# Kernel tuning notes

Hardware: AMD Instinct MI355X
Metric: run time of the kernel (lower is better)

The kernel has to match this reference:

```python
import jax, jax.numpy as jnp
import numpy as np

B, H, FEAT = 16384, 256, 256
GX, GY, SW = 70, 70, 2


def setup_inputs() -> dict:
    key = jax.random.key(0)
    ks = jax.random.split(key, 10)
    stdv = 1.0 / np.sqrt(H)
    feats = jax.random.normal(ks[0], (B, FEAT), dtype=jnp.float32)
    coords = jax.random.randint(ks[1], (B, 2), 0, 64).astype(jnp.float32)
    input_tensor = jnp.concatenate([feats, coords], axis=1)  # [B, FEAT+2]
    hidden = jax.random.normal(ks[2], (B, H), dtype=jnp.float32)
    u = lambda k, shp: jax.random.uniform(k, shp, jnp.float32, -stdv, stdv)
    return {
        "input_tensor": input_tensor,
        "hidden": hidden,
        "w_ih": u(ks[3], (4 * H, FEAT)),
        "b_ih": u(ks[4], (4 * H,)),
        "w_hh": u(ks[5], (4 * H, H)),
        "b_hh": u(ks[6], (4 * H,)),
        "w_out": u(ks[7], (H, 2 * H)),
        "b_out": u(ks[8], (H,)),
        "memory": jax.random.normal(ks[9], (GX, GY, H), dtype=jnp.float32) * 0.1,
    }


def reference(input_tensor, hidden, w_ih, b_ih, w_hh, b_hh, w_out, b_out, memory):
    feature = input_tensor[:, :-2]
    grid = input_tensor[:, -2:].astype(jnp.int32) + SW  # [B,2]

    gi = feature @ w_ih.T + b_ih  # [B,4H]
    gh = hidden @ w_hh.T + b_hh   # [B,4H]
    i_r, i_i, i_n, i_s = jnp.split(gi, 4, axis=1)
    h_r, h_i, h_n, h_s = jnp.split(gh, 4, axis=1)

    resetgate = jax.nn.sigmoid(i_r + h_r)
    updategate = jax.nn.sigmoid(i_i + h_i)
    spatialgate = jax.nn.sigmoid(i_s + h_s)
    newgate = jnp.tanh(i_n + resetgate * h_n)

    # gather (2*SW+1)^2 neighborhood per sample from spatial memory
    gx = jnp.clip(grid[:, 0], 0, GX - 1)
    gy = jnp.clip(grid[:, 1], 0, GY - 1)
    off = jnp.arange(-SW, SW + 1)  # [K]
    xi = jnp.clip(gx[:, None] + off[None, :], 0, GX - 1)  # [B,K]
    yi = jnp.clip(gy[:, None] + off[None, :], 0, GY - 1)  # [B,K]
    K = 2 * SW + 1
    x_flat = jnp.broadcast_to(xi[:, :, None], (xi.shape[0], K, K)).reshape(xi.shape[0], -1)
    y_flat = jnp.broadcast_to(yi[:, None, :], (yi.shape[0], K, K)).reshape(yi.shape[0], -1)
    context = memory[x_flat, y_flat]  # [B, K*K, H]

    # attention (query is detached in original)
    q = jax.lax.stop_gradient(newgate)  # [B,H]
    attn = jnp.einsum('bh,bkh->bk', q, context)  # [B, K*K]
    attn = jnp.where(attn == 0, -jnp.inf, attn)
    w = jax.nn.softmax(attn, axis=1)
    w = jnp.where(jnp.isnan(w), 0.0, w)
    mix = jnp.einsum('bk,bkh->bh', w, context)  # [B,H]
    combined = jnp.concatenate([mix, q], axis=1)  # [B,2H]
    atten_cs = jnp.tanh(combined @ w_out.T + b_out)  # [B,H]

    curr_state = newgate + spatialgate * atten_cs
    output = curr_state + updategate * (hidden - curr_state)
    return output
```

## Files before the change

### kernel.cpp

```cpp
#include <hip/hip_runtime.h>
#include <stdint.h>

#define B_N 16384
#define H_N 256
#define IN_W 258
#define GX_N 70
#define GY_N 70
#define SW_N 2
#define KK_N 25

typedef __bf16 bf16x8 __attribute__((ext_vector_type(8)));
typedef __bf16 bf16x4 __attribute__((ext_vector_type(4)));
typedef __bf16 bf16x2 __attribute__((ext_vector_type(2)));
typedef float f32x4 __attribute__((ext_vector_type(4)));
typedef float f32x2 __attribute__((ext_vector_type(2)));

#define AS1 __attribute__((address_space(1)))
#define AS3 __attribute__((address_space(3)))

static __device__ __forceinline__ void gload16(const void* g, void* l) {
    __builtin_amdgcn_global_load_lds((const AS1 uint32_t*)g, (AS3 uint32_t*)l, 16, 0, 0);
}

#define E_AB   8388608ULL
#define E_WF   8912896ULL
#define E_WOUT 9043968ULL
#define E_COMB 9043968ULL
#define E_UGSG 17432576ULL

__global__ __launch_bounds__(256) void cast_kernel(
    const float* __restrict__ in_t, const float* __restrict__ hid,
    const float* __restrict__ wih, const float* __restrict__ whh,
    const float* __restrict__ wout, __bf16* __restrict__ dst)
{
    size_t g = (size_t)blockIdx.x * blockDim.x + threadIdx.x;
    size_t stride = (size_t)gridDim.x * blockDim.x;
    for (size_t e = g * 4; e < E_WOUT; e += stride * 4) {
        bf16x4 o;
        if (e < E_AB) {
            size_t row = e >> 9;
            size_t c = e & 511;
            if (c < 256) {
                const f32x2* s2 = reinterpret_cast<const f32x2*>(in_t + row * IN_W + c);
                f32x2 a = s2[0], b = s2[1];
                o.x = (__bf16)a.x; o.y = (__bf16)a.y;
                o.z = (__bf16)b.x; o.w = (__bf16)b.y;
            } else {
                f32x4 v = *reinterpret_cast<const f32x4*>(hid + row * 256 + (c - 256));
                o.x = (__bf16)v.x; o.y = (__bf16)v.y;
                o.z = (__bf16)v.z; o.w = (__bf16)v.w;
            }
        } else if (e < E_WF) {
            size_t off = e - E_AB;
            size_t j = off >> 9;
            size_t k = off & 511;
            size_t c = j >> 8;
            size_t col = j & 255;
            size_t base = (c == 0) ? 0 : (c == 1) ? 256 : (c == 2) ? 768 : 512;
            const float* srcm = (k < 256) ? wih : whh;
            f32x4 v = *reinterpret_cast<const f32x4*>(srcm + (base + col) * 256 + (k & 255));
            o.x = (__bf16)v.x; o.y = (__bf16)v.y;
            o.z = (__bf16)v.z; o.w = (__bf16)v.w;
        } else {
            f32x4 v = *reinterpret_cast<const f32x4*>(wout + (e - E_WF));
            o.x = (__bf16)v.x; o.y = (__bf16)v.y;
            o.z = (__bf16)v.z; o.w = (__bf16)v.w;
        }
        *reinterpret_cast<bf16x4*>(dst + e) = o;
    }
}

__global__ __launch_bounds__(256, 2) void gates_gemm(
    const __bf16* __restrict__ AB, const __bf16* __restrict__ wfull,
    const float* __restrict__ b_ih, const float* __restrict__ b_hh,
    __bf16* __restrict__ comb, __bf16* __restrict__ ugsg)
{
    __shared__ __bf16 ldsA[2][4096];
    __shared__ __bf16 ldsB[2][4096];
    const int t = threadIdx.x;
    const int lane = t & 63, w = t >> 6;
    const int lr = lane & 15, seg = lane >> 4;
    const int rb = blockIdx.x * 128;
    const int h0 = blockIdx.y * 32;

    const int rA = t & 127;
    const int sA = t >> 7;
    const __bf16* gAt = AB + (size_t)(rb + rA) * 512 + sA * 8;
    const int bc = rA >> 5, bcol = rA & 31;
    const __bf16* gBt = wfull + (size_t)(bc * 256 + h0 + bcol) * 512 + sA * 8;
    __bf16* lA0 = &ldsA[0][t * 8];
    __bf16* lA1 = &ldsA[1][t * 8];
    __bf16* lB0 = &ldsB[0][t * 8];
    __bf16* lB1 = &ldsB[1][t * 8];

    f32x4 acc[2][6], accni[2][2], accnh[2][2];
#pragma unroll
    for (int rh = 0; rh < 2; rh++) {
#pragma unroll
        for (int cn = 0; cn < 6; cn++) acc[rh][cn] = (f32x4){0.f, 0.f, 0.f, 0.f};
        accni[rh][0] = (f32x4){0.f, 0.f, 0.f, 0.f};
        accni[rh][1] = (f32x4){0.f, 0.f, 0.f, 0.f};
        accnh[rh][0] = (f32x4){0.f, 0.f, 0.f, 0.f};
        accnh[rh][1] = (f32x4){0.f, 0.f, 0.f, 0.f};
    }

    gload16(gAt + 0, lA0);
    gload16(gAt + 16, lA0 + 2048);
    gload16(gBt + 0, lB0);
    gload16(gBt + 16, lB0 + 2048);
    __syncthreads();

#pragma unroll 1
    for (int tt = 0; tt < 16; tt++) {
        const int cur = tt & 1;
        if (tt < 15) {
            const int kn = (tt + 1) * 32;
            __bf16* la = cur ? lA0 : lA1;
            __bf16* lb = cur ? lB0 : lB1;
            gload16(gAt + kn, la);
            gload16(gAt + kn + 16, la + 2048);
            gload16(gBt + kn, lb);
            gload16(gBt + kn + 16, lb + 2048);
        }
        const __bf16* cA = ldsA[cur];
        const __bf16* cB = ldsB[cur];
        bf16x8 af[2];
#pragma unroll
        for (int rh = 0; rh < 2; rh++)
            af[rh] = *reinterpret_cast<const bf16x8*>(cA + seg * 1024 + (w * 32 + rh * 16 + lr) * 8);
#pragma unroll
        for (int cn = 0; cn < 6; cn++) {
            const int c = cn >> 1, hh = cn & 1;
            bf16x8 bb = *reinterpret_cast<const bf16x8*>(cB + seg * 1024 + (c * 32 + hh * 16 + lr) * 8);
#pragma unroll
            for (int rh = 0; rh < 2; rh++)
                acc[rh][(c << 1) + hh] = __builtin_amdgcn_mfma_f32_16x16x32_bf16(af[rh], bb, acc[rh][(c << 1) + hh], 0, 0, 0);
        }
        bf16x8 b6 = *reinterpret_cast<const bf16x8*>(cB + seg * 1024 + (96 + lr) * 8);
        bf16x8 b7 = *reinterpret_cast<const bf16x8*>(cB + seg * 1024 + (112 + lr) * 8);
        if (tt < 8) {
#pragma unroll
            for (int rh = 0; rh < 2; rh++) {
                accni[rh][0] = __builtin_amdgcn_mfma_f32_16x16x32_bf16(af[rh], b6, accni[rh][0], 0, 0, 0);
                accni[rh][1] = __builtin_amdgcn_mfma_f32_16x16x32_bf16(af[rh], b7, accni[rh][1], 0, 0, 0);
            }
        } else {
#pragma unroll
            for (int rh = 0; rh < 2; rh++) {
                accnh[rh][0] = __builtin_amdgcn_mfma_f32_16x16x32_bf16(af[rh], b6, accnh[rh][0], 0, 0, 0);
                accnh[rh][1] = __builtin_amdgcn_mfma_f32_16x16x32_bf16(af[rh], b7, accnh[rh][1], 0, 0, 0);
            }
        }
        __syncthreads();
    }

#pragma unroll
    for (int hh = 0; hh < 2; hh++) {
        const int col = h0 + hh * 16 + lr;
        const float br_ = b_ih[col] + b_hh[col];
        const float bi_ = b_ih[col + 256] + b_hh[col + 256];
        const float bs_ = b_ih[col + 768] + b_hh[col + 768];
        const float bni = b_ih[col + 512];
        const float bnh = b_hh[col + 512];
#pragma unroll
        for (int rh = 0; rh < 2; rh++) {
#pragma unroll
            for (int r = 0; r < 4; r++) {
                const int row = rb + w * 32 + rh * 16 + seg * 4 + r;
                float sr = acc[rh][hh][r] + br_;
                float si = acc[rh][2 + hh][r] + bi_;
                float ss = acc[rh][4 + hh][r] + bs_;
                float vni = accni[rh][hh][r] + bni;
                float vnh = accnh[rh][hh][r] + bnh;
                float rg = 1.f / (1.f + __expf(-sr));
                float ug = 1.f / (1.f + __expf(-si));
                float sg = 1.f / (1.f + __expf(-ss));
                float ng = tanhf(vni + rg * vnh);
                comb[(size_t)row * 512 + 256 + col] = (__bf16)ng;
                bf16x2 us;
                us.x = (__bf16)ug;
                us.y = (__bf16)sg;
                *reinterpret_cast<bf16x2*>(ugsg + ((size_t)row * 256 + col) * 2) = us;
            }
        }
    }
}

__global__ __launch_bounds__(256) void attn_kernel(
    const float* __restrict__ in_t, const float* __restrict__ memory,
    __bf16* __restrict__ comb)
{
    const int w = threadIdx.x >> 6;
    const int lane = threadIdx.x & 63;
    const int b = blockIdx.x * 4 + w;
    const float* row_in = in_t + (size_t)b * IN_W;
    int gx = (int)row_in[256] + SW_N;
    int gy = (int)row_in[257] + SW_N;
    gx = min(max(gx, 0), GX_N - 1);
    gy = min(max(gy, 0), GY_N - 1);

    bf16x4 qb = *reinterpret_cast<const bf16x4*>(comb + (size_t)b * 512 + 256 + lane * 4);
    float q0 = (float)qb.x, q1 = (float)qb.y, q2 = (float)qb.z, q3 = (float)qb.w;

    float m = -INFINITY, d = 0.f;
    float o0 = 0.f, o1 = 0.f, o2 = 0.f, o3 = 0.f;
#pragma unroll
    for (int k = 0; k < KK_N; k++) {
        int i = k / 5, j = k % 5;
        int xi = min(max(gx + i - SW_N, 0), GX_N - 1);
        int yj = min(max(gy + j - SW_N, 0), GY_N - 1);
        const f32x4* cp = reinterpret_cast<const f32x4*>(memory + ((size_t)xi * GY_N + yj) * H_N);
        f32x4 v = cp[lane];
        float p = q0 * v.x + q1 * v.y + q2 * v.z + q3 * v.w;
        for (int off = 32; off; off >>= 1) p += __shfl_xor(p, off, 64);
        float a = (p == 0.f) ? -INFINITY : p;
        float mn = fmaxf(m, a);
        if (mn != -INFINITY) {
            float alpha = __expf(m - mn);
            float e = __expf(a - mn);
            d = d * alpha + e;
            o0 = o0 * alpha + e * v.x;
            o1 = o1 * alpha + e * v.y;
            o2 = o2 * alpha + e * v.z;
            o3 = o3 * alpha + e * v.w;
            m = mn;
        }
    }
    float inv = (d != 0.f) ? 1.f / d : 0.f;
    bf16x4 ob;
    ob.x = (__bf16)(o0 * inv);
    ob.y = (__bf16)(o1 * inv);
    ob.z = (__bf16)(o2 * inv);
    ob.w = (__bf16)(o3 * inv);
    *reinterpret_cast<bf16x4*>(comb + (size_t)b * 512 + lane * 4) = ob;
}

__global__ __launch_bounds__(256) void out_gemm(
    const __bf16* __restrict__ comb, const __bf16* __restrict__ woB,
    const float* __restrict__ b_out, const __bf16* __restrict__ ugsg,
    const float* __restrict__ hidden, float* __restrict__ out)
{
    __shared__ __bf16 ldsA[2][4096];
    __shared__ __bf16 ldsB[2][2048];
    const int t = threadIdx.x;
    const int lane = t & 63, w = t >> 6;
    const int lr = lane & 15, seg = lane >> 4;
    const int rb = blockIdx.x * 128;
    const int n0 = blockIdx.y * 64;

    const __bf16* gAt = comb + (size_t)(rb + (t & 127)) * 512 + ((t >> 7) << 3);
    const __bf16* gBt = woB + (size_t)(n0 + (t & 63)) * 512 + ((t >> 6) << 3);
    __bf16* lA0 = &ldsA[0][t * 8];
    __bf16* lA1 = &ldsA[1][t * 8];
    __bf16* lB0 = &ldsB[0][t * 8];
    __bf16* lB1 = &ldsB[1][t * 8];

    f32x4 acc[2][4];
#pragma unroll
    for (int rh = 0; rh < 2; rh++)
#pragma unroll
        for (int ct = 0; ct < 4; ct++) acc[rh][ct] = (f32x4){0.f, 0.f, 0.f, 0.f};

    gload16(gAt + 0, lA0);
    gload16(gAt + 16, lA0 + 2048);
    gload16(gBt + 0, lB0);
    __syncthreads();

#pragma unroll 1
    for (int tt = 0; tt < 16; tt++) {
        const int cur = tt & 1;
        if (tt < 15) {
            const int kn = (tt + 1) * 32;
            __bf16* la = cur ? lA0 : lA1;
            __bf16* lb = cur ? lB0 : lB1;
            gload16(gAt + kn, la);
            gload16(gAt + kn + 16, la + 2048);
            gload16(gBt + kn, lb);
        }
        const __bf16* cA = ldsA[cur];
        const __bf16* cB = ldsB[cur];
        bf16x8 af[2];
#pragma unroll
        for (int rh = 0; rh < 2; rh++)
            af[rh] = *reinterpret_cast<const bf16x8*>(cA + seg * 1024 + (w * 32 + rh * 16 + lr) * 8);
#pragma unroll
        for (int ct = 0; ct < 4; ct++) {
            bf16x8 bb = *reinterpret_cast<const bf16x8*>(cB + seg * 512 + (ct * 16 + lr) * 8);
#pragma unroll
            for (int rh = 0; rh < 2; rh++)
                acc[rh][ct] = __builtin_amdgcn_mfma_f32_16x16x32_bf16(af[rh], bb, acc[rh][ct], 0, 0, 0);
        }
        __syncthreads();
    }

#pragma unroll
    for (int ct = 0; ct < 4; ct++) {
        int col = n0 + ct * 16 + lr;
        float bo = b_out[col];
#pragma unroll
        for (int rh = 0; rh < 2; rh++) {
#pragma unroll
            for (int r = 0; r < 4; r++) {
                int row = rb + w * 32 + rh * 16 + seg * 4 + r;
                size_t idx = (size_t)row * 256 + col;
                float acs = tanhf(acc[rh][ct][r] + bo);
                float ng = (float)comb[(size_t)row * 512 + 256 + col];
                bf16x2 us = *reinterpret_cast<const bf16x2*>(ugsg + idx * 2);
                float ug = (float)us.x, sg = (float)us.y;
                float curr = ng + sg * acs;
                out[idx] = curr + ug * (hidden[idx] - curr);
            }
        }
    }
}

extern "C" void kernel_launch(void* const* d_in, const int* in_sizes, int n_in,
                              void* d_out, int out_size, void* d_ws, size_t ws_size,
                              hipStream_t stream) {
    const float* input_t = (const float*)d_in[0];
    const float* hidden  = (const float*)d_in[1];
    const float* w_ih    = (const float*)d_in[2];
    const float* b_ih    = (const float*)d_in[3];
    const float* w_hh    = (const float*)d_in[4];
    const float* b_hh    = (const float*)d_in[5];
    const float* w_out   = (const float*)d_in[6];
    const float* b_out   = (const float*)d_in[7];
    const float* memory  = (const float*)d_in[8];
    float* out = (float*)d_out;

    __bf16* base  = (__bf16*)d_ws;
    __bf16* AB    = base;
    __bf16* wfull = base + E_AB;
    __bf16* woutB = base + E_WF;
    __bf16* comb  = base + E_COMB;
    __bf16* ugsg  = base + E_UGSG;

    cast_kernel<<<4096, 256, 0, stream>>>(input_t, hidden, w_ih, w_hh, w_out, base);
    gates_gemm<<<dim3(128, 8), 256, 0, stream>>>(AB, wfull, b_ih, b_hh, comb, ugsg);
    attn_kernel<<<4096, 256, 0, stream>>>(input_t, memory, comb);
    out_gemm<<<dim3(128, 4), 256, 0, stream>>>(comb, woutB, b_out, ugsg, hidden, out);
}
```

Measured before the change: 204.1 us.

## Triple-buffer LDS in both GEMMs with vmcnt waits and MFMA priority

Both GEMM kernels move from double-buffered to triple-buffered LDS staging. Each iteration now waits on an explicit vmcnt count and a single barrier, then issues the load two tiles ahead, replacing the trailing __syncthreads. The MFMA section is wrapped in s_setprio to favour math waves. The min-blocks-per-CU hint on gates_gemm is dropped, and each block uses more LDS, which may lower occupancy. Correctness depends on the hand-counted vmcnt values matching the number of outstanding global-to-LDS loads.

```diff
diff --git a/kernel.cpp b/kernel.cpp
--- a/kernel.cpp
+++ b/kernel.cpp
@@ -70,13 +70,13 @@
     }
 }
 
-__global__ __launch_bounds__(256, 2) void gates_gemm(
+__global__ __launch_bounds__(256) void gates_gemm(
     const __bf16* __restrict__ AB, const __bf16* __restrict__ wfull,
     const float* __restrict__ b_ih, const float* __restrict__ b_hh,
     __bf16* __restrict__ comb, __bf16* __restrict__ ugsg)
 {
-    __shared__ __bf16 ldsA[2][4096];
-    __shared__ __bf16 ldsB[2][4096];
+    __shared__ __bf16 ldsA[3][4096];
+    __shared__ __bf16 ldsB[3][4096];
     const int t = threadIdx.x;
     const int lane = t & 63, w = t >> 6;
     const int lr = lane & 15, seg = lane >> 4;
@@ -88,10 +88,6 @@
     const __bf16* gAt = AB + (size_t)(rb + rA) * 512 + sA * 8;
     const int bc = rA >> 5, bcol = rA & 31;
     const __bf16* gBt = wfull + (size_t)(bc * 256 + h0 + bcol) * 512 + sA * 8;
-    __bf16* lA0 = &ldsA[0][t * 8];
-    __bf16* lA1 = &ldsA[1][t * 8];
-    __bf16* lB0 = &ldsB[0][t * 8];
-    __bf16* lB1 = &ldsB[1][t * 8];
 
     f32x4 acc[2][6], accni[2][2], accnh[2][2];
 #pragma unroll
@@ -104,30 +100,36 @@
         accnh[rh][1] = (f32x4){0.f, 0.f, 0.f, 0.f};
     }
 
-    gload16(gAt + 0, lA0);
-    gload16(gAt + 16, lA0 + 2048);
-    gload16(gBt + 0, lB0);
-    gload16(gBt + 16, lB0 + 2048);
-    __syncthreads();
-
+#define G_STAGE(TILE, BUF)                                \
+    do {                                                  \
+        const int kn_ = (TILE) * 32;                      \
+        __bf16* la_ = &ldsA[(BUF)][t * 8];                \
+        __bf16* lb_ = &ldsB[(BUF)][t * 8];                \
+        gload16(gAt + kn_, la_);                          \
+        gload16(gAt + kn_ + 16, la_ + 2048);              \
+        gload16(gBt + kn_, lb_);                          \
+        gload16(gBt + kn_ + 16, lb_ + 2048);              \
+    } while (0)
+
+    G_STAGE(0, 0);
+    G_STAGE(1, 1);
+
+    int cur = 0, nxt2 = 2;
 #pragma unroll 1
     for (int tt = 0; tt < 16; tt++) {
-        const int cur = tt & 1;
-        if (tt < 15) {
-            const int kn = (tt + 1) * 32;
-            __bf16* la = cur ? lA0 : lA1;
-            __bf16* lb = cur ? lB0 : lB1;
-            gload16(gAt + kn, la);
-            gload16(gAt + kn + 16, la + 2048);
-            gload16(gBt + kn, lb);
-            gload16(gBt + kn + 16, lb + 2048);
-        }
+        if (tt < 15) asm volatile("s_waitcnt vmcnt(4)" ::: "memory");
+        else         asm volatile("s_waitcnt vmcnt(0)" ::: "memory");
+        __builtin_amdgcn_s_barrier();
+        if (tt < 14) G_STAGE(tt + 2, nxt2);
+
         const __bf16* cA = ldsA[cur];
         const __bf16* cB = ldsB[cur];
         bf16x8 af[2];
 #pragma unroll
         for (int rh = 0; rh < 2; rh++)
             af[rh] = *reinterpret_cast<const bf16x8*>(cA + seg * 1024 + (w * 32 + rh * 16 + lr) * 8);
+
+        __builtin_amdgcn_s_setprio(1);
 #pragma unroll
         for (int cn = 0; cn < 6; cn++) {
             const int c = cn >> 1, hh = cn & 1;
@@ -151,8 +153,12 @@
                 accnh[rh][1] = __builtin_amdgcn_mfma_f32_16x16x32_bf16(af[rh], b7, accnh[rh][1], 0, 0, 0);
             }
         }
-        __syncthreads();
-    }
+        __builtin_amdgcn_s_setprio(0);
+
+        cur = (cur == 2) ? 0 : cur + 1;
+        nxt2 = (nxt2 == 2) ? 0 : nxt2 + 1;
+    }
+#undef G_STAGE
 
 #pragma unroll
     for (int hh = 0; hh < 2; hh++) {
@@ -240,8 +246,8 @@
     const float* __restrict__ b_out, const __bf16* __restrict__ ugsg,
     const float* __restrict__ hidden, float* __restrict__ out)
 {
-    __shared__ __bf16 ldsA[2][4096];
-    __shared__ __bf16 ldsB[2][2048];
+    __shared__ __bf16 ldsA[3][4096];
+    __shared__ __bf16 ldsB[3][2048];
     const int t = threadIdx.x;
     const int lane = t & 63, w = t >> 6;
     const int lr = lane & 15, seg = lane >> 4;
@@ -250,10 +256,6 @@
 
     const __bf16* gAt = comb + (size_t)(rb + (t & 127)) * 512 + ((t >> 7) << 3);
     const __bf16* gBt = woB + (size_t)(n0 + (t & 63)) * 512 + ((t >> 6) << 3);
-    __bf16* lA0 = &ldsA[0][t * 8];
-    __bf16* lA1 = &ldsA[1][t * 8];
-    __bf16* lB0 = &ldsB[0][t * 8];
-    __bf16* lB1 = &ldsB[1][t * 8];
 
     f32x4 acc[2][4];
 #pragma unroll
@@ -261,28 +263,34 @@
 #pragma unroll
         for (int ct = 0; ct < 4; ct++) acc[rh][ct] = (f32x4){0.f, 0.f, 0.f, 0.f};
 
-    gload16(gAt + 0, lA0);
-    gload16(gAt + 16, lA0 + 2048);
-    gload16(gBt + 0, lB0);
-    __syncthreads();
-
+#define O_STAGE(TILE, BUF)                                \
+    do {                                                  \
+        const int kn_ = (TILE) * 32;                      \
+        __bf16* la_ = &ldsA[(BUF)][t * 8];                \
+        __bf16* lb_ = &ldsB[(BUF)][t * 8];                \
+        gload16(gAt + kn_, la_);                          \
+        gload16(gAt + kn_ + 16, la_ + 2048);              \
+        gload16(gBt + kn_, lb_);                          \
+    } while (0)
+
+    O_STAGE(0, 0);
+    O_STAGE(1, 1);
+
+    int cur = 0, nxt2 = 2;
 #pragma unroll 1
     for (int tt = 0; tt < 16; tt++) {
-        const int cur = tt & 1;
-        if (tt < 15) {
-            const int kn = (tt + 1) * 32;
-            __bf16* la = cur ? lA0 : lA1;
-            __bf16* lb = cur ? lB0 : lB1;
-            gload16(gAt + kn, la);
-            gload16(gAt + kn + 16, la + 2048);
-            gload16(gBt + kn, lb);
-        }
+        if (tt < 15) asm volatile("s_waitcnt vmcnt(3)" ::: "memory");
+        else         asm volatile("s_waitcnt vmcnt(0)" ::: "memory");
+        __builtin_amdgcn_s_barrier();
+        if (tt < 14) O_STAGE(tt + 2, nxt2);
+
         const __bf16* cA = ldsA[cur];
         const __bf16* cB = ldsB[cur];
         bf16x8 af[2];
 #pragma unroll
         for (int rh = 0; rh < 2; rh++)
             af[rh] = *reinterpret_cast<const bf16x8*>(cA + seg * 1024 + (w * 32 + rh * 16 + lr) * 8);
+        __builtin_amdgcn_s_setprio(1);
 #pragma unroll
         for (int ct = 0; ct < 4; ct++) {
             bf16x8 bb = *reinterpret_cast<const bf16x8*>(cB + seg * 512 + (ct * 16 + lr) * 8);
@@ -290,8 +298,12 @@
             for (int rh = 0; rh < 2; rh++)
                 acc[rh][ct] = __builtin_amdgcn_mfma_f32_16x16x32_bf16(af[rh], bb, acc[rh][ct], 0, 0, 0);
         }
-        __syncthreads();
-    }
+        __builtin_amdgcn_s_setprio(0);
+
+        cur = (cur == 2) ? 0 : cur + 1;
+        nxt2 = (nxt2 == 2) ? 0 : nxt2 + 1;
+    }
+#undef O_STAGE
 
 #pragma unroll
     for (int ct = 0; ct < 4; ct++) {
```

After: 211.0 us. 1.03x slower.

## Compute attention scores per-lane instead of via wave-wide shuffle reductions

Applied to the files above, without the earlier changes.

Restructures the attention kernel into three phases. First, 50 lanes each compute half of one of the 25 neighbor dot products from a query staged in LDS, reduced with a single shuffle. Next comes a two-pass softmax on the scores, and finally a second pass re-reads the context rows to form the weighted sum. This removes the 25 serialized 6-step shuffle reductions and the per-step online-softmax rescaling, at the cost of reading each context row twice, uncoalesced strided loads in the score phase, and block-wide barriers.

```diff
diff --git a/kernel.cpp b/kernel.cpp
--- a/kernel.cpp
+++ b/kernel.cpp
@@ -190,6 +190,8 @@
     const float* __restrict__ in_t, const float* __restrict__ memory,
     __bf16* __restrict__ comb)
 {
+    __shared__ __bf16 qlds[4][256];
+    __shared__ float sclds[4][32];
     const int w = threadIdx.x >> 6;
     const int lane = threadIdx.x & 63;
     const int b = blockIdx.x * 4 + w;
@@ -200,38 +202,59 @@
     gy = min(max(gy, 0), GY_N - 1);
 
     bf16x4 qb = *reinterpret_cast<const bf16x4*>(comb + (size_t)b * 512 + 256 + lane * 4);
-    float q0 = (float)qb.x, q1 = (float)qb.y, q2 = (float)qb.z, q3 = (float)qb.w;
-
-    float m = -INFINITY, d = 0.f;
-    float o0 = 0.f, o1 = 0.f, o2 = 0.f, o3 = 0.f;
+    *reinterpret_cast<bf16x4*>(&qlds[w][lane * 4]) = qb;
+    __syncthreads();
+
+    if (lane < 50) {
+        const int k = lane >> 1, half = lane & 1;
+        const int i = k / 5, j = k - i * 5;
+        const int xi = min(max(gx + i - SW_N, 0), GX_N - 1);
+        const int yj = min(max(gy + j - SW_N, 0), GY_N - 1);
+        const float* vp = memory + ((size_t)xi * GY_N + yj) * H_N + half * 128;
+        const __bf16* qp = &qlds[w][half * 128];
+        float s = 0.f;
+#pragma unroll
+        for (int mq = 0; mq < 32; mq++) {
+            f32x4 v = *reinterpret_cast<const f32x4*>(vp + mq * 4);
+            bf16x4 qq = *reinterpret_cast<const bf16x4*>(qp + mq * 4);
+            s += (float)qq.x * v.x + (float)qq.y * v.y + (float)qq.z * v.z + (float)qq.w * v.w;
+        }
+        s += __shfl_xor(s, 1, 64);
+        if (half == 0) sclds[w][k] = s;
+    }
+    __syncthreads();
+
+    float sc[KK_N];
 #pragma unroll
     for (int k = 0; k < KK_N; k++) {
-        int i = k / 5, j = k % 5;
-        int xi = min(max(gx + i - SW_N, 0), GX_N - 1);
-        int yj = min(max(gy + j - SW_N, 0), GY_N - 1);
-        const f32x4* cp = reinterpret_cast<const f32x4*>(memory + ((size_t)xi * GY_N + yj) * H_N);
-        f32x4 v = cp[lane];
-        float p = q0 * v.x + q1 * v.y + q2 * v.z + q3 * v.w;
-        for (int off = 32; off; off >>= 1) p += __shfl_xor(p, off, 64);
-        float a = (p == 0.f) ? -INFINITY : p;
-        float mn = fmaxf(m, a);
-        if (mn != -INFINITY) {
-            float alpha = __expf(m - mn);
-            float e = __expf(a - mn);
-            d = d * alpha + e;
-            o0 = o0 * alpha + e * v.x;
-            o1 = o1 * alpha + e * v.y;
-            o2 = o2 * alpha + e * v.z;
-            o3 = o3 * alpha + e * v.w;
-            m = mn;
-        }
-    }
-    float inv = (d != 0.f) ? 1.f / d : 0.f;
+        float a = sclds[w][k];
+        sc[k] = (a == 0.f) ? -INFINITY : a;
+    }
+    float mx = -INFINITY;
+#pragma unroll
+    for (int k = 0; k < KK_N; k++) mx = fmaxf(mx, sc[k]);
+    float d = 0.f;
+    if (mx > -INFINITY) {
+#pragma unroll
+        for (int k = 0; k < KK_N; k++) { sc[k] = __expf(sc[k] - mx); d += sc[k]; }
+    } else {
+#pragma unroll
+        for (int k = 0; k < KK_N; k++) sc[k] = 0.f;
+    }
+    const float inv = (d != 0.f) ? 1.f / d : 0.f;
+
+    f32x4 o = (f32x4){0.f, 0.f, 0.f, 0.f};
+#pragma unroll
+    for (int k = 0; k < KK_N; k++) {
+        const int i = k / 5, j = k % 5;
+        const int xi = min(max(gx + i - SW_N, 0), GX_N - 1);
+        const int yj = min(max(gy + j - SW_N, 0), GY_N - 1);
+        f32x4 v = *reinterpret_cast<const f32x4*>(memory + ((size_t)xi * GY_N + yj) * H_N + lane * 4);
+        const float wk = sc[k] * inv;
+        o.x += wk * v.x; o.y += wk * v.y; o.z += wk * v.z; o.w += wk * v.w;
+    }
     bf16x4 ob;
-    ob.x = (__bf16)(o0 * inv);
-    ob.y = (__bf16)(o1 * inv);
-    ob.z = (__bf16)(o2 * inv);
-    ob.w = (__bf16)(o3 * inv);
+    ob.x = (__bf16)o.x; ob.y = (__bf16)o.y; ob.z = (__bf16)o.z; ob.w = (__bf16)o.w;
     *reinterpret_cast<bf16x4*>(comb + (size_t)b * 512 + lane * 4) = ob;
 }
 
```

Result: slower. 233.2 us (+14.3%).
